# Optimization experiments

Hardware: AMD Instinct MI355X
Metric: run time of the kernel (lower is better)

The kernel has to match this reference:

```python
import jax, jax.numpy as jnp
import numpy as np

TEMPERATURE = 5.0

def setup_inputs() -> dict:
    key = jax.random.key(0)
    k1, k2 = jax.random.split(key)
    B, D = 8192, 128
    features = jax.random.normal(k1, (B, D), dtype=jnp.float32)
    labels = jax.random.randint(k2, (B,), 0, 100, dtype=jnp.int64)
    return {"features": features, "labels": labels, "fac_label": 3}


def reference(features, labels, fac_label):
    # features: [B, D], labels: [B]
    B = features.shape[0]
    # positive-pair mask; note original's mask_scale row-copy loop is a no-op,
    # so mask_scale == mask, and mask_cross_feature == ones (fac_label unused in effect)
    mask = (labels[:, None] == labels[None, :]).astype(features.dtype)  # [B, B]

    sim = jnp.matmul(features, features.T) / TEMPERATURE  # [B, B]
    logits_max = jax.lax.stop_gradient(jnp.max(sim, axis=1, keepdims=True))
    logits = sim - logits_max

    # remove self-contrast (diagonal)
    logits_mask = 1.0 - jnp.eye(B, dtype=features.dtype)
    mask = mask * logits_mask

    exp_logits = jnp.exp(logits) * logits_mask
    log_prob = logits - jnp.log(1e-12 + exp_logits.sum(axis=1, keepdims=True))

    mean_log_prob_pos_mask = (mask * log_prob).sum(axis=1)  # [B]
    # vectorized form of the per-element reciprocal loop: 1/count where count>0 else 0
    cnt = mask.sum(axis=1)
    recip = jnp.where(cnt == 0, 0.0, 1.0 / jnp.where(cnt == 0, 1.0, cnt))

    loss = -(mean_log_prob_pos_mask * recip).mean()
    return loss
```

## Files before the change

### kernel.cpp

```cpp
#include <hip/hip_runtime.h>


#define BN 8192
#define DK 128
#define INV_T 0.2f

#define CHUNKS 8
#define CHUNK_COLS (BN / CHUNKS)
#define ROWS_PER_BLOCK 128
#define RT_PER_WAVE 2

typedef __attribute__((ext_vector_type(8))) short bf16x8;
typedef __attribute__((ext_vector_type(4))) float f32x4;

__device__ __forceinline__ unsigned short f2bf(float f) {
    unsigned u = __builtin_bit_cast(unsigned, f);
    u += 0x7fffu + ((u >> 16) & 1u);
    return (unsigned short)(u >> 16);
}

__global__ __launch_bounds__(256) void cast_kernel(const float* __restrict__ F,
                                                   unsigned short* __restrict__ Fb) {
    int idx = blockIdx.x * 256 + threadIdx.x;
    float4 v = ((const float4*)F)[idx];
    ushort4 o;
    o.x = f2bf(v.x); o.y = f2bf(v.y); o.z = f2bf(v.z); o.w = f2bf(v.w);
    ((ushort4*)Fb)[idx] = o;
}

__global__ __launch_bounds__(256) void supcon_main(const short* __restrict__ Fb,
                                                   const int* __restrict__ labels,
                                                   float4* __restrict__ part) {
    const int t    = threadIdx.x;
    const int wave = t >> 6;
    const int lane = t & 63;
    const int quad = lane >> 4;
    const int l16  = lane & 15;
    const int rowBase = blockIdx.x * ROWS_PER_BLOCK + wave * (RT_PER_WAVE * 16);
    const int colBase = blockIdx.y * CHUNK_COLS;

    bf16x8 a[RT_PER_WAVE][4];
#pragma unroll
    for (int rt = 0; rt < RT_PER_WAVE; ++rt)
#pragma unroll
        for (int kt = 0; kt < 4; ++kt)
            a[rt][kt] = *(const bf16x8*)(Fb + (size_t)(rowBase + rt * 16 + l16) * DK
                                            + kt * 32 + quad * 8);

    int   rlbl[RT_PER_WAVE][4], irow[RT_PER_WAVE][4];
    float m[RT_PER_WAVE][4], Z[RT_PER_WAVE][4], A[RT_PER_WAVE][4], C[RT_PER_WAVE][4];
#pragma unroll
    for (int rt = 0; rt < RT_PER_WAVE; ++rt)
#pragma unroll
        for (int r = 0; r < 4; ++r) {
            irow[rt][r] = rowBase + rt * 16 + quad * 4 + r;
            rlbl[rt][r] = labels[irow[rt][r]];
            m[rt][r] = -__builtin_inff();
            Z[rt][r] = 0.f; A[rt][r] = 0.f; C[rt][r] = 0.f;
        }

    for (int jt = 0; jt < CHUNK_COLS / 16; ++jt) {
        const int j0 = colBase + jt * 16;
        bf16x8 b[4];
#pragma unroll
        for (int kt = 0; kt < 4; ++kt)
            b[kt] = *(const bf16x8*)(Fb + (size_t)(j0 + l16) * DK + kt * 32 + quad * 8);
        const int jcol = j0 + l16;
        const int clbl = labels[jcol];

#pragma unroll
        for (int rt = 0; rt < RT_PER_WAVE; ++rt) {
            f32x4 acc = {0.f, 0.f, 0.f, 0.f};
#pragma unroll
            for (int kt = 0; kt < 4; ++kt)
                acc = __builtin_amdgcn_mfma_f32_16x16x32_bf16(a[rt][kt], b[kt], acc, 0, 0, 0);

#pragma unroll
            for (int r = 0; r < 4; ++r) {
                float s    = acc[r] * INV_T;
                bool  diag = (jcol == irow[rt][r]);
                float mo   = m[rt][r];
                float mn   = fmaxf(mo, s);
                float zs   = Z[rt][r];
                if (mn > mo) zs *= __expf(mo - mn);
                float e = __expf(s - mn);
                zs += diag ? 0.f : e;
                Z[rt][r] = zs;
                m[rt][r] = mn;
                bool match = (!diag) && (clbl == rlbl[rt][r]);
                A[rt][r] += match ? s : 0.f;
                C[rt][r] += match ? 1.f : 0.f;
            }
        }
    }

#pragma unroll
    for (int rt = 0; rt < RT_PER_WAVE; ++rt)
#pragma unroll
        for (int r = 0; r < 4; ++r) {
            float mm = m[rt][r], zz = Z[rt][r], aa = A[rt][r], cc = C[rt][r];
#pragma unroll
            for (int h = 1; h < 16; h <<= 1) {
                float om = __shfl_xor(mm, h);
                float oz = __shfl_xor(zz, h);
                float oa = __shfl_xor(aa, h);
                float oc = __shfl_xor(cc, h);
                float mn = fmaxf(mm, om);
                zz = zz * __expf(mm - mn) + oz * __expf(om - mn);
                mm = mn; aa += oa; cc += oc;
            }
            if (l16 == 0)
                part[(size_t)blockIdx.y * BN + irow[rt][r]] = make_float4(mm, zz, aa, cc);
        }
}

__global__ __launch_bounds__(256) void supcon_finalize(const float4* __restrict__ part,
                                                       float* __restrict__ bsums) {
    const int i = blockIdx.x * 256 + threadIdx.x;
    float mm = -__builtin_inff(), zz = 0.f, aa = 0.f, cc = 0.f;
#pragma unroll
    for (int c = 0; c < CHUNKS; ++c) {
        float4 p = part[(size_t)c * BN + i];
        float mn = fmaxf(mm, p.x);
        zz = zz * __expf(mm - mn) + p.y * __expf(p.x - mn);
        mm = mn; aa += p.z; cc += p.w;
    }
    float term = 0.f;
    if (cc > 0.5f) term = (aa - cc * mm) / cc - __logf(1e-12f + zz);

    float sum = term;
#pragma unroll
    for (int h = 1; h < 64; h <<= 1) sum += __shfl_xor(sum, h);
    __shared__ float ss[4];
    if ((threadIdx.x & 63) == 0) ss[threadIdx.x >> 6] = sum;
    __syncthreads();
    if (threadIdx.x == 0) bsums[blockIdx.x] = ss[0] + ss[1] + ss[2] + ss[3];
}

__global__ void supcon_final(const float* __restrict__ bsums, float* __restrict__ out) {
    float v = (threadIdx.x < 32) ? bsums[threadIdx.x] : 0.f;
#pragma unroll
    for (int h = 1; h < 64; h <<= 1) v += __shfl_xor(v, h);
    if (threadIdx.x == 0) out[0] = -v * (1.0f / BN);
}

extern "C" void kernel_launch(void* const* d_in, const int* in_sizes, int n_in,
                              void* d_out, int out_size, void* d_ws, size_t ws_size,
                              hipStream_t stream) {
    const float* F      = (const float*)d_in[0];
    const int*   labels = (const int*)d_in[1];
    float* out = (float*)d_out;
    char*  ws  = (char*)d_ws;

    unsigned short* Fb   = (unsigned short*)ws;
    float4*         part = (float4*)(ws + (size_t)2 * 1024 * 1024);
    float*          bsum = (float*)(ws + (size_t)3 * 1024 * 1024);

    cast_kernel<<<(BN * DK / 4) / 256, 256, 0, stream>>>(F, Fb);
    supcon_main<<<dim3(BN / ROWS_PER_BLOCK, CHUNKS), 256, 0, stream>>>((const short*)Fb,
                                                                       labels, part);
    supcon_finalize<<<BN / 256, 256, 0, stream>>>(part, bsum);
    supcon_final<<<1, 64, 0, stream>>>(bsum, out);
}
```

Baseline: 130.6 us.

## Replace per-pair positive sums with class-sum dot products and fixed-offset exp

```diff
diff --git a/kernel.cpp b/kernel.cpp
--- a/kernel.cpp
+++ b/kernel.cpp
@@ -4,11 +4,28 @@
 #define BN 8192
 #define DK 128
 #define INV_T 0.2f
-
-#define CHUNKS 8
-#define CHUNK_COLS (BN / CHUNKS)
-#define ROWS_PER_BLOCK 128
-#define RT_PER_WAVE 2
+#define C1F 0.28853901f
+#define C40F 27.7258872f
+
+#define CHUNKS 32
+#define CCOLS (BN / CHUNKS)
+#define RPB 256
+#define RT 4
+#define NJT (CCOLS / 16)
+
+#define NCLS 100
+#define PB 128
+#define PROWS (BN / PB)
+
+#define OFF_FB    0
+#define OFF_DIAG  (2 * 1024 * 1024)
+#define OFF_PART  (OFF_DIAG + 32768)
+#define OFF_GP    (OFF_PART + 2 * 1024 * 1024)
+#define OFF_HISTP (OFF_GP + PB * NCLS * DK * 4)
+#define OFF_G     (OFF_HISTP + PB * NCLS * 4)
+#define OFF_HIST  (OFF_G + NCLS * DK * 4)
+#define OFF_BSUM  (OFF_HIST + 512)
+#define OFF_CTR   (OFF_BSUM + 128)
 
 typedef __attribute__((ext_vector_type(8))) short bf16x8;
 typedef __attribute__((ext_vector_type(4))) float f32x4;
@@ -19,129 +36,246 @@
     return (unsigned short)(u >> 16);
 }
 
-__global__ __launch_bounds__(256) void cast_kernel(const float* __restrict__ F,
-                                                   unsigned short* __restrict__ Fb) {
-    int idx = blockIdx.x * 256 + threadIdx.x;
-    float4 v = ((const float4*)F)[idx];
-    ushort4 o;
-    o.x = f2bf(v.x); o.y = f2bf(v.y); o.z = f2bf(v.z); o.w = f2bf(v.w);
-    ((ushort4*)Fb)[idx] = o;
-}
-
-__global__ __launch_bounds__(256) void supcon_main(const short* __restrict__ Fb,
+__device__ __forceinline__ float fexp2(float x) {
+#if __has_builtin(__builtin_amdgcn_exp2f)
+    return __builtin_amdgcn_exp2f(x);
+#else
+    float r; asm("v_exp_f32 %0, %1" : "=v"(r) : "v"(x)); return r;
+#endif
+}
+
+__global__ __launch_bounds__(256) void prep_kernel(const float* __restrict__ F,
                                                    const int* __restrict__ labels,
-                                                   float4* __restrict__ part) {
+                                                   unsigned short* __restrict__ Fb,
+                                                   float* __restrict__ diag,
+                                                   float* __restrict__ Gp,
+                                                   int* __restrict__ histp,
+                                                   unsigned int* __restrict__ ctr) {
+    const int t  = threadIdx.x;
+    const int b  = blockIdx.x;
+    const int r0 = b * PROWS;
+
+    if (b == 0 && t == 0) *ctr = 0u;
+
+    const float4* F4  = (const float4*)F + (size_t)b * (PROWS * DK / 4);
+    ushort4*      Fb4 = (ushort4*)Fb + (size_t)b * (PROWS * DK / 4);
+#pragma unroll
+    for (int k = 0; k < PROWS * DK / 4 / 256; ++k) {
+        float4 v = F4[k * 256 + t];
+        ushort4 o;
+        o.x = f2bf(v.x); o.y = f2bf(v.y); o.z = f2bf(v.z); o.w = f2bf(v.w);
+        Fb4[k * 256 + t] = o;
+    }
+
+    {
+        const int row = r0 + (t >> 2);
+        const int q   = t & 3;
+        const float4* rp = (const float4*)(F + (size_t)row * DK) + q * 8;
+        float s = 0.f;
+#pragma unroll
+        for (int k = 0; k < 8; ++k) {
+            float4 v = rp[k];
+            s += v.x * v.x + v.y * v.y + v.z * v.z + v.w * v.w;
+        }
+        s += __shfl_xor(s, 1);
+        s += __shfl_xor(s, 2);
+        if (q == 0) diag[row] = s;
+    }
+
+    __shared__ int   lh[NCLS];
+    __shared__ float gl[NCLS][DK];
+    float* glf = (float*)gl;
+    if (t < NCLS) lh[t] = 0;
+#pragma unroll
+    for (int k = 0; k < NCLS * DK / 256; ++k) glf[k * 256 + t] = 0.f;
+    __syncthreads();
+
+    if (t < PROWS) atomicAdd(&lh[labels[r0 + t]], 1);
+
+    if (t < DK) {
+        for (int rr = 0; rr < PROWS; ++rr) {
+            const int row = r0 + rr;
+            const int c   = labels[row];
+            gl[c][t] += F[(size_t)row * DK + t];
+        }
+    }
+    __syncthreads();
+
+    if (t < NCLS) histp[b * NCLS + t] = lh[t];
+#pragma unroll
+    for (int k = 0; k < NCLS * DK / 256; ++k) {
+        const int idx = k * 256 + t;
+        Gp[(size_t)b * (NCLS * DK) + idx] = glf[idx];
+    }
+}
+
+template <bool DIAGBLK>
+__device__ __forceinline__ void supcon_rows(const short* __restrict__ Fb,
+                                            float2* __restrict__ part,
+                                            int bx, int by) {
     const int t    = threadIdx.x;
-    const int wave = t >> 6;
-    const int lane = t & 63;
-    const int quad = lane >> 4;
-    const int l16  = lane & 15;
-    const int rowBase = blockIdx.x * ROWS_PER_BLOCK + wave * (RT_PER_WAVE * 16);
-    const int colBase = blockIdx.y * CHUNK_COLS;
-
-    bf16x8 a[RT_PER_WAVE][4];
-#pragma unroll
-    for (int rt = 0; rt < RT_PER_WAVE; ++rt)
+    const int wave = t >> 6, lane = t & 63;
+    const int quad = lane >> 4, l16 = lane & 15;
+    const int rowBase = bx * RPB + wave * (RT * 16);
+    const int colBase = by * CCOLS;
+
+    bf16x8 a[RT][4];
+#pragma unroll
+    for (int rt = 0; rt < RT; ++rt)
 #pragma unroll
         for (int kt = 0; kt < 4; ++kt)
             a[rt][kt] = *(const bf16x8*)(Fb + (size_t)(rowBase + rt * 16 + l16) * DK
                                             + kt * 32 + quad * 8);
 
-    int   rlbl[RT_PER_WAVE][4], irow[RT_PER_WAVE][4];
-    float m[RT_PER_WAVE][4], Z[RT_PER_WAVE][4], A[RT_PER_WAVE][4], C[RT_PER_WAVE][4];
-#pragma unroll
-    for (int rt = 0; rt < RT_PER_WAVE; ++rt)
+    float mr[RT][4], Zs[RT][4];
+#pragma unroll
+    for (int rt = 0; rt < RT; ++rt)
+#pragma unroll
+        for (int r = 0; r < 4; ++r) { mr[rt][r] = -__builtin_inff(); Zs[rt][r] = 0.f; }
+
+    const short* bp = Fb + (size_t)(colBase + l16) * DK + quad * 8;
+    bf16x8 bc[4], bn[4];
+#pragma unroll
+    for (int kt = 0; kt < 4; ++kt) bc[kt] = *(const bf16x8*)(bp + kt * 32);
+
+    auto STEP = [&](const bf16x8 (&bb)[4], int jtc) {
+        const int j0 = colBase + jtc * 16;
+#pragma unroll
+        for (int rt = 0; rt < RT; ++rt) {
+            f32x4 acc = {0.f, 0.f, 0.f, 0.f};
+#pragma unroll
+            for (int kt = 0; kt < 4; ++kt)
+                acc = __builtin_amdgcn_mfma_f32_16x16x32_bf16(a[rt][kt], bb[kt], acc, 0, 0, 0);
+            float e[4];
+#pragma unroll
+            for (int r = 0; r < 4; ++r) {
+                const float raw = acc[r];
+                mr[rt][r] = fmaxf(mr[rt][r], raw);
+                e[r] = fexp2(fmaf(raw, C1F, -40.0f));
+            }
+            if (DIAGBLK) {
+                const int irow0 = rowBase + rt * 16 + quad * 4;
+#pragma unroll
+                for (int r = 0; r < 4; ++r)
+                    if (j0 + l16 == irow0 + r) e[r] = 0.f;
+            }
+#pragma unroll
+            for (int r = 0; r < 4; ++r) Zs[rt][r] += e[r];
+        }
+    };
+
+    for (int jt = 0; jt < NJT; jt += 2) {
+        bp += 16 * DK;
+#pragma unroll
+        for (int kt = 0; kt < 4; ++kt) bn[kt] = *(const bf16x8*)(bp + kt * 32);
+        STEP(bc, jt);
+        if (jt + 2 < NJT) {
+            bp += 16 * DK;
+#pragma unroll
+            for (int kt = 0; kt < 4; ++kt) bc[kt] = *(const bf16x8*)(bp + kt * 32);
+        }
+        STEP(bn, jt + 1);
+    }
+
+#pragma unroll
+    for (int rt = 0; rt < RT; ++rt)
 #pragma unroll
         for (int r = 0; r < 4; ++r) {
-            irow[rt][r] = rowBase + rt * 16 + quad * 4 + r;
-            rlbl[rt][r] = labels[irow[rt][r]];
-            m[rt][r] = -__builtin_inff();
-            Z[rt][r] = 0.f; A[rt][r] = 0.f; C[rt][r] = 0.f;
-        }
-
-    for (int jt = 0; jt < CHUNK_COLS / 16; ++jt) {
-        const int j0 = colBase + jt * 16;
-        bf16x8 b[4];
-#pragma unroll
-        for (int kt = 0; kt < 4; ++kt)
-            b[kt] = *(const bf16x8*)(Fb + (size_t)(j0 + l16) * DK + kt * 32 + quad * 8);
-        const int jcol = j0 + l16;
-        const int clbl = labels[jcol];
-
-#pragma unroll
-        for (int rt = 0; rt < RT_PER_WAVE; ++rt) {
-            f32x4 acc = {0.f, 0.f, 0.f, 0.f};
-#pragma unroll
-            for (int kt = 0; kt < 4; ++kt)
-                acc = __builtin_amdgcn_mfma_f32_16x16x32_bf16(a[rt][kt], b[kt], acc, 0, 0, 0);
-
-#pragma unroll
-            for (int r = 0; r < 4; ++r) {
-                float s    = acc[r] * INV_T;
-                bool  diag = (jcol == irow[rt][r]);
-                float mo   = m[rt][r];
-                float mn   = fmaxf(mo, s);
-                float zs   = Z[rt][r];
-                if (mn > mo) zs *= __expf(mo - mn);
-                float e = __expf(s - mn);
-                zs += diag ? 0.f : e;
-                Z[rt][r] = zs;
-                m[rt][r] = mn;
-                bool match = (!diag) && (clbl == rlbl[rt][r]);
-                A[rt][r] += match ? s : 0.f;
-                C[rt][r] += match ? 1.f : 0.f;
-            }
-        }
-    }
-
-#pragma unroll
-    for (int rt = 0; rt < RT_PER_WAVE; ++rt)
-#pragma unroll
-        for (int r = 0; r < 4; ++r) {
-            float mm = m[rt][r], zz = Z[rt][r], aa = A[rt][r], cc = C[rt][r];
+            float mm = mr[rt][r], zz = Zs[rt][r];
 #pragma unroll
             for (int h = 1; h < 16; h <<= 1) {
-                float om = __shfl_xor(mm, h);
-                float oz = __shfl_xor(zz, h);
-                float oa = __shfl_xor(aa, h);
-                float oc = __shfl_xor(cc, h);
-                float mn = fmaxf(mm, om);
-                zz = zz * __expf(mm - mn) + oz * __expf(om - mn);
-                mm = mn; aa += oa; cc += oc;
+                mm = fmaxf(mm, __shfl_xor(mm, h));
+                zz += __shfl_xor(zz, h);
             }
             if (l16 == 0)
-                part[(size_t)blockIdx.y * BN + irow[rt][r]] = make_float4(mm, zz, aa, cc);
-        }
-}
-
-__global__ __launch_bounds__(256) void supcon_finalize(const float4* __restrict__ part,
-                                                       float* __restrict__ bsums) {
-    const int i = blockIdx.x * 256 + threadIdx.x;
-    float mm = -__builtin_inff(), zz = 0.f, aa = 0.f, cc = 0.f;
-#pragma unroll
+                part[(size_t)by * BN + rowBase + rt * 16 + quad * 4 + r] =
+                    make_float2(mm, zz);
+        }
+}
+
+__global__ __launch_bounds__(256, 3) void supcon_main(const short* __restrict__ Fb,
+                                                      float2* __restrict__ part,
+                                                      const float* __restrict__ Gp,
+                                                      const int* __restrict__ histp,
+                                                      float* __restrict__ G,
+                                                      int* __restrict__ hist) {
+    if (blockIdx.y == CHUNKS) {
+        const int base = blockIdx.x * 256 + threadIdx.x;
+        for (int idx = base; idx < NCLS * DK + NCLS; idx += BN) {
+            if (idx < NCLS * DK) {
+                float s = 0.f;
+#pragma unroll 8
+                for (int p = 0; p < PB; ++p) s += Gp[(size_t)p * (NCLS * DK) + idx];
+                G[idx] = s;
+            } else {
+                const int c = idx - NCLS * DK;
+                int s = 0;
+#pragma unroll 8
+                for (int p = 0; p < PB; ++p) s += histp[p * NCLS + c];
+                hist[c] = s;
+            }
+        }
+        return;
+    }
+    if (blockIdx.x == blockIdx.y) supcon_rows<true >(Fb, part, blockIdx.x, blockIdx.y);
+    else                          supcon_rows<false>(Fb, part, blockIdx.x, blockIdx.y);
+}
+
+__global__ __launch_bounds__(256) void supcon_finalize(const float* __restrict__ F,
+                                                       const int* __restrict__ labels,
+                                                       const float2* __restrict__ part,
+                                                       const float* __restrict__ diag,
+                                                       const float* __restrict__ G,
+                                                       const int* __restrict__ hist,
+                                                       float* __restrict__ bsums,
+                                                       unsigned int* __restrict__ ctr,
+                                                       float* __restrict__ out) {
+    const int t = threadIdx.x;
+    const int i = blockIdx.x * 256 + t;
+
+    float mraw = -__builtin_inff(), Zm = 0.f;
+#pragma unroll 8
     for (int c = 0; c < CHUNKS; ++c) {
-        float4 p = part[(size_t)c * BN + i];
-        float mn = fmaxf(mm, p.x);
-        zz = zz * __expf(mm - mn) + p.y * __expf(p.x - mn);
-        mm = mn; aa += p.z; cc += p.w;
-    }
+        const float2 p = part[(size_t)c * BN + i];
+        mraw = fmaxf(mraw, p.x);
+        Zm += p.y;
+    }
+    const int   lbl = labels[i];
+    const float cnt = (float)(hist[lbl] - 1);
+
+    const float4* fr = (const float4*)(F + (size_t)i * DK);
+    const float4* gr = (const float4*)(G + lbl * DK);
+    float dot = 0.f;
+#pragma unroll 8
+    for (int k = 0; k < DK / 4; ++k) {
+        const float4 av = fr[k], gv = gr[k];
+        dot += av.x * gv.x + av.y * gv.y + av.z * gv.z + av.w * gv.w;
+    }
+
+    const float m = mraw * INV_T;
+    const float A = (dot - diag[i]) * INV_T;
     float term = 0.f;
-    if (cc > 0.5f) term = (aa - cc * mm) / cc - __logf(1e-12f + zz);
+    if (cnt > 0.5f)
+        term = (A - cnt * m) / cnt - __logf(1e-12f + Zm * __expf(C40F - m));
 
     float sum = term;
 #pragma unroll
     for (int h = 1; h < 64; h <<= 1) sum += __shfl_xor(sum, h);
     __shared__ float ss[4];
-    if ((threadIdx.x & 63) == 0) ss[threadIdx.x >> 6] = sum;
+    if ((t & 63) == 0) ss[t >> 6] = sum;
     __syncthreads();
-    if (threadIdx.x == 0) bsums[blockIdx.x] = ss[0] + ss[1] + ss[2] + ss[3];
-}
-
-__global__ void supcon_final(const float* __restrict__ bsums, float* __restrict__ out) {
-    float v = (threadIdx.x < 32) ? bsums[threadIdx.x] : 0.f;
-#pragma unroll
-    for (int h = 1; h < 64; h <<= 1) v += __shfl_xor(v, h);
-    if (threadIdx.x == 0) out[0] = -v * (1.0f / BN);
+    if (t == 0) {
+        bsums[blockIdx.x] = ss[0] + ss[1] + ss[2] + ss[3];
+        __threadfence();
+        const unsigned old = atomicAdd(ctr, 1u);
+        if (old == (BN / 256) - 1) {
+            __threadfence();
+            float tot = 0.f;
+            const volatile float* vb = bsums;
+            for (int c = 0; c < BN / 256; ++c) tot += vb[c];
+            out[0] = -tot * (1.0f / BN);
+        }
+    }
 }
 
 extern "C" void kernel_launch(void* const* d_in, const int* in_sizes, int n_in,
@@ -152,13 +286,19 @@
     float* out = (float*)d_out;
     char*  ws  = (char*)d_ws;
 
-    unsigned short* Fb   = (unsigned short*)ws;
-    float4*         part = (float4*)(ws + (size_t)2 * 1024 * 1024);
-    float*          bsum = (float*)(ws + (size_t)3 * 1024 * 1024);
-
-    cast_kernel<<<(BN * DK / 4) / 256, 256, 0, stream>>>(F, Fb);
-    supcon_main<<<dim3(BN / ROWS_PER_BLOCK, CHUNKS), 256, 0, stream>>>((const short*)Fb,
-                                                                       labels, part);
-    supcon_finalize<<<BN / 256, 256, 0, stream>>>(part, bsum);
-    supcon_final<<<1, 64, 0, stream>>>(bsum, out);
-}
+    unsigned short* Fb    = (unsigned short*)(ws + OFF_FB);
+    float*          diag  = (float*)(ws + OFF_DIAG);
+    float2*         part  = (float2*)(ws + OFF_PART);
+    float*          Gp    = (float*)(ws + OFF_GP);
+    int*            histp = (int*)(ws + OFF_HISTP);
+    float*          G     = (float*)(ws + OFF_G);
+    int*            hist  = (int*)(ws + OFF_HIST);
+    float*          bsums = (float*)(ws + OFF_BSUM);
+    unsigned int*   ctr   = (unsigned int*)(ws + OFF_CTR);
+
+    prep_kernel<<<PB, 256, 0, stream>>>(F, labels, Fb, diag, Gp, histp, ctr);
+    supcon_main<<<dim3(BN / RPB, CHUNKS + 1), 256, 0, stream>>>((const short*)Fb, part,
+                                                                Gp, histp, G, hist);
+    supcon_finalize<<<BN / 256, 256, 0, stream>>>(F, labels, part, diag, G, hist,
+                                                  bsums, ctr, out);
+}
```

Result: no change. 129.0 us (-1.2%).
